# Kernel tuning notes

Measured on AMD Instinct MI355X. Metric: run time of the kernel, lower is better.

## Reference

```python
import jax, jax.numpy as jnp
import numpy as np

EPS = 1e-8
TAU = 1.0


def graph_conv(h_in, adj, W, b):
    # h: [N, D_out]
    h = h_in @ W
    nrm = jnp.linalg.norm(h, axis=1, keepdims=True)
    h_norm = h / jnp.maximum(nrm, EPS)  # F.normalize with eps clamp
    # cosine-sim logits + log-adjacency mask -> row softmax
    logits = (h_norm @ h_norm.T) / TAU + jnp.log(adj + EPS)  # [N, N]
    attn = jax.nn.softmax(logits, axis=1)
    return attn @ h + b


def setup_inputs() -> dict:
    key = jax.random.key(0)
    ks = jax.random.split(key, 20)
    N, F, H, C = 4096, 512, 128, 16

    def xavier(k, fan_in, fan_out):
        s = float(np.sqrt(6.0 / (fan_in + fan_out)))
        return jax.random.uniform(k, (fan_in, fan_out), minval=-s, maxval=s, dtype=jnp.float32)

    return {
        "x": jax.random.normal(ks[0], (N, F), dtype=jnp.float32),
        "adj_low": jax.random.uniform(ks[1], (N, N), dtype=jnp.float32),
        "adj_high": jax.random.uniform(ks[2], (N, N), dtype=jnp.float32),
        "adj_mid": jax.random.uniform(ks[3], (N, N), dtype=jnp.float32),
        "w_low0": xavier(ks[4], F, H), "b_low0": jnp.zeros((H,), jnp.float32),
        "w_high0": xavier(ks[5], F, H), "b_high0": jnp.zeros((H,), jnp.float32),
        "w_mid0": xavier(ks[6], F, H), "b_mid0": jnp.zeros((H,), jnp.float32),
        "w_low1": xavier(ks[7], H, C), "b_low1": jnp.zeros((C,), jnp.float32),
        "w_high1": xavier(ks[8], H, C), "b_high1": jnp.zeros((C,), jnp.float32),
        "w_mid1": xavier(ks[9], H, C), "b_mid1": jnp.zeros((C,), jnp.float32),
        "g0": jnp.ones((3,), jnp.float32),
        "g1": jnp.ones((3,), jnp.float32),
    }


def reference(x, adj_low, adj_high, adj_mid,
              w_low0, b_low0, w_high0, b_high0, w_mid0, b_mid0,
              w_low1, b_low1, w_high1, b_high1, w_mid1, b_mid1,
              g0, g1):
    # layer 0 (inner layer: ReLU; dropout p=0 in eval mode -> identity)
    hl = jax.nn.relu(graph_conv(x, adj_low, w_low0, b_low0))
    hh = jax.nn.relu(graph_conv(x, adj_high, w_high0, b_high0))
    hm = jax.nn.relu(graph_conv(x, adj_mid, w_mid0, b_mid0))
    w = jax.nn.softmax(g0)
    h = w[0] * hl + w[1] * hh + w[2] * hm

    # layer 1 (final layer: no activation)
    hl = graph_conv(h, adj_low, w_low1, b_low1)
    hh = graph_conv(h, adj_high, w_high1, b_high1)
    hm = graph_conv(h, adj_mid, w_mid1, b_mid1)
    w = jax.nn.softmax(g1)
    h = w[0] * hl + w[1] * hh + w[2] * hm

    return jax.nn.log_softmax(h, axis=-1)
```

## Files before the change

### kernel.cpp

```cpp
#include <hip/hip_runtime.h>

#define N_NODES 4096
#define F_IN 512
#define H_DIM 128
#define C_DIM 16
#define EPSF 1e-8f
#define LOG2E 1.4426950408889634f
#define SMAX 2.0f
#define NKS0 8
#define KLEN0 (N_NODES / NKS0)
#define NT0 (KLEN0 / 32)
#define NKS1 8

typedef __attribute__((ext_vector_type(8))) short bf16x8;
typedef __attribute__((ext_vector_type(4))) short bf16x4;
typedef __attribute__((ext_vector_type(4))) float f32x4;

__device__ __forceinline__ ushort f2bf(float f){
  union { float f; unsigned u; } v; v.f = f;
  unsigned u = v.u;
  return (ushort)((u + 0x7fffu + ((u >> 16) & 1u)) >> 16);
}
__device__ __forceinline__ float bf2f(ushort h){
  union { unsigned u; float f; } v; v.u = ((unsigned)h) << 16;
  return v.f;
}

__global__ __launch_bounds__(256) void proj0_kernel(
    const float* __restrict__ x,
    const float* __restrict__ Wl, const float* __restrict__ Wh,
    const float* __restrict__ Wm,
    ushort* __restrict__ hn, ushort* __restrict__ hvT)
{
  const int t = threadIdx.x;
  const int d = t & 127;
  const int half = t >> 7;
  const int r0 = blockIdx.x * 8;
  __shared__ float xs[8][F_IN];
  for (int i = t; i < 8 * F_IN; i += 256)
    xs[i >> 9][i & 511] = x[(size_t)(r0 + (i >> 9)) * F_IN + (i & 511)];
  __syncthreads();

  float acc0[8], acc1[8], acc2[8];
#pragma unroll
  for (int r = 0; r < 8; r++) { acc0[r] = 0.f; acc1[r] = 0.f; acc2[r] = 0.f; }

  const int k0 = half * (F_IN / 2);
  for (int k = k0; k < k0 + F_IN / 2; k++) {
    float wl = Wl[k * H_DIM + d];
    float wh = Wh[k * H_DIM + d];
    float wm = Wm[k * H_DIM + d];
#pragma unroll
    for (int r = 0; r < 8; r++) {
      float xv = xs[r][k];
      acc0[r] = fmaf(xv, wl, acc0[r]);
      acc1[r] = fmaf(xv, wh, acc1[r]);
      acc2[r] = fmaf(xv, wm, acc2[r]);
    }
  }

  __shared__ float part[3][8][128];
  if (half == 1) {
#pragma unroll
    for (int r = 0; r < 8; r++) {
      part[0][r][d] = acc0[r]; part[1][r][d] = acc1[r]; part[2][r][d] = acc2[r];
    }
  }
  __syncthreads();
  if (half == 0) {
#pragma unroll
    for (int r = 0; r < 8; r++) {
      acc0[r] += part[0][r][d]; acc1[r] += part[1][r][d]; acc2[r] += part[2][r][d];
    }
  }

  __shared__ float red[24][2];
  const int wv = t >> 6;
  const int lane = t & 63;

#define REDUCE_BRANCH(ACC, B)                                        \
  _Pragma("unroll")                                                  \
  for (int r = 0; r < 8; r++) {                                      \
    float v = ACC[r] * ACC[r];                                       \
    v += __shfl_down(v, 32); v += __shfl_down(v, 16);                \
    v += __shfl_down(v, 8);  v += __shfl_down(v, 4);                 \
    v += __shfl_down(v, 2);  v += __shfl_down(v, 1);                 \
    if (lane == 0) red[(B) * 8 + r][wv] = v;                         \
  }
  if (half == 0) {
    REDUCE_BRANCH(acc0, 0)
    REDUCE_BRANCH(acc1, 1)
    REDUCE_BRANCH(acc2, 2)
  }
  __syncthreads();

#define WRITE_BRANCH(ACC, B)                                                   \
  _Pragma("unroll")                                                            \
  for (int r = 0; r < 8; r++) {                                                \
    float nrm = sqrtf(red[(B) * 8 + r][0] + red[(B) * 8 + r][1]);              \
    float rn = 1.0f / fmaxf(nrm, EPSF);                                        \
    float h = ACC[r];                                                          \
    hn[((size_t)(B) * N_NODES + r0 + r) * H_DIM + d] = f2bf(h * rn);           \
    hvT[((size_t)(B) * H_DIM + d) * N_NODES + r0 + r] = f2bf(h);               \
  }
  if (half == 0) {
    WRITE_BRANCH(acc0, 0)
    WRITE_BRANCH(acc1, 1)
    WRITE_BRANCH(acc2, 2)
  }
#undef REDUCE_BRANCH
#undef WRITE_BRANCH
}

__global__ __launch_bounds__(512) void flash0_kernel(
    const ushort* __restrict__ hn, const ushort* __restrict__ hvT,
    const float* __restrict__ adj_l, const float* __restrict__ adj_h,
    const float* __restrict__ adj_m,
    float* __restrict__ pl0, ushort* __restrict__ pO)
{
  const int tid = threadIdx.x;
  const int w = tid >> 6;
  const int lane = tid & 63;
  const int lr = lane & 15;
  const int lg = lane >> 4;
  const int ks = blockIdx.y;
  const int b = blockIdx.z;
  const int q0 = blockIdx.x * 128 + w * 16;
  const float* adj = (b == 0) ? adj_l : (b == 1) ? adj_h : adj_m;
  const ushort* Qg = hn + (size_t)b * N_NODES * H_DIM;
  const ushort* VTg = hvT + (size_t)b * H_DIM * N_NODES;
  const int kbase = ks * KLEN0;

  __shared__ ushort sK[2][32 * 128];
  __shared__ ushort sV[2][128 * 32];
  __shared__ ushort pbuf[8][16][40];

  bf16x8 qf[4];
  {
    const ushort* qp = Qg + (size_t)(q0 + lr) * H_DIM + lg * 8;
#pragma unroll
    for (int u = 0; u < 4; u++) qf[u] = *(const bf16x8*)(qp + 32 * u);
  }

  f32x4 o[8];
#pragma unroll
  for (int dt = 0; dt < 8; dt++) o[dt] = (f32x4){0.f, 0.f, 0.f, 0.f};
  float lsum[4] = {0.f, 0.f, 0.f, 0.f};

  const int qrow_base = q0 + lg * 4;
  const float* ar[4];
#pragma unroll
  for (int r = 0; r < 4; r++)
    ar[r] = adj + (size_t)(qrow_base + r) * N_NODES + kbase;

  const int kk = tid >> 4, kc = tid & 15;
  const size_t kOff = (size_t)kk * H_DIM + ((size_t)(kc ^ (kk & 7)) << 3);
  const int dV = tid >> 2, vc = tid & 3;
  const size_t vOff = (size_t)dV * N_NODES + ((size_t)(vc ^ ((dV >> 1) & 3)) << 3);

#define STAGE(BUF, K0)                                                         \
  {                                                                            \
    const ushort* ksrc = Qg + (size_t)(K0) * H_DIM;                            \
    const ushort* vsrc = VTg + (K0);                                           \
    __builtin_amdgcn_global_load_lds(ksrc + kOff,                              \
        (char*)&sK[BUF][0] + w * 1024, 16, 0, 0);                              \
    __builtin_amdgcn_global_load_lds(vsrc + vOff,                              \
        (char*)&sV[BUF][0] + w * 1024, 16, 0, 0);                              \
  }

  STAGE(0, kbase)

  float a0c[4], a1c[4];
#pragma unroll
  for (int r = 0; r < 4; r++) { a0c[r] = ar[r][lr]; a1c[r] = ar[r][16 + lr]; }

  for (int t = 0; t < NT0; t++) {
    const int cur = t & 1;
    __syncthreads();
    if (t + 1 < NT0) STAGE(cur ^ 1, kbase + (t + 1) * 32)

    float a0n[4], a1n[4];
    if (t + 1 < NT0) {
#pragma unroll
      for (int r = 0; r < 4; r++) {
        a0n[r] = ar[r][(t + 1) * 32 + lr];
        a1n[r] = ar[r][(t + 1) * 32 + 16 + lr];
      }
    }

    f32x4 s0 = (f32x4){0.f, 0.f, 0.f, 0.f};
    f32x4 s1 = (f32x4){0.f, 0.f, 0.f, 0.f};
    const char* sKc = (const char*)&sK[cur][0];
#pragma unroll
    for (int u = 0; u < 4; u++) {
      const int c0 = lg + 4 * u;
      bf16x8 kf0 = *(const bf16x8*)(sKc + lr * 256 + ((c0 ^ (lr & 7)) << 4));
      bf16x8 kf1 = *(const bf16x8*)(sKc + (lr + 16) * 256 + ((c0 ^ (lr & 7)) << 4));
      s0 = __builtin_amdgcn_mfma_f32_16x16x32_bf16(qf[u], kf0, s0, 0, 0, 0);
      s1 = __builtin_amdgcn_mfma_f32_16x16x32_bf16(qf[u], kf1, s1, 0, 0, 0);
    }
    float p0[4], p1[4];
#pragma unroll
    for (int r = 0; r < 4; r++) {
      float e0 = exp2f(fmaf(s0[r], LOG2E, -SMAX));
      float e1 = exp2f(fmaf(s1[r], LOG2E, -SMAX));
      p0[r] = e0 * (a0c[r] + EPSF);
      p1[r] = e1 * (a1c[r] + EPSF);
      lsum[r] += p0[r] + p1[r];
    }
#pragma unroll
    for (int r = 0; r < 4; r++) {
      pbuf[w][lg * 4 + r][lr]      = f2bf(p0[r]);
      pbuf[w][lg * 4 + r][16 + lr] = f2bf(p1[r]);
    }
    bf16x8 pf = *(const bf16x8*)&pbuf[w][lr][lg * 8];
    const char* sVc = (const char*)&sV[cur][0];
#pragma unroll
    for (int dt = 0; dt < 8; dt++) {
      const int dd = dt * 16 + lr;
      bf16x8 vf = *(const bf16x8*)(sVc + dd * 64 + ((lg ^ ((dd >> 1) & 3)) << 4));
      o[dt] = __builtin_amdgcn_mfma_f32_16x16x32_bf16(pf, vf, o[dt], 0, 0, 0);
    }
#pragma unroll
    for (int r = 0; r < 4; r++) { a0c[r] = a0n[r]; a1c[r] = a1n[r]; }
  }
#undef STAGE

  const int ps = b * NKS0 + ks;
#pragma unroll
  for (int r = 0; r < 4; r++) {
    const size_t row = (size_t)ps * N_NODES + qrow_base + r;
    float psum = lsum[r];
#pragma unroll
    for (int dd = 1; dd < 16; dd <<= 1) psum += __shfl_xor(psum, dd);
    if (lr == 0) pl0[row] = psum;
#pragma unroll
    for (int dt = 0; dt < 8; dt++)
      pO[row * H_DIM + dt * 16 + lr] = f2bf(o[dt][r]);
  }
}

__global__ __launch_bounds__(128) void mix1_kernel(
    const float* __restrict__ pl0, const ushort* __restrict__ pO,
    const float* __restrict__ bl0, const float* __restrict__ bh0,
    const float* __restrict__ bm0,
    const float* __restrict__ Wl1, const float* __restrict__ Wh1,
    const float* __restrict__ Wm1,
    const float* __restrict__ g0,
    ushort* __restrict__ hn1b, ushort* __restrict__ hbT)
{
  const int q = blockIdx.x;
  const int t = threadIdx.x;
  float ga = g0[0], gb = g0[1], gc = g0[2];
  float gm = fmaxf(ga, fmaxf(gb, gc));
  float e0 = expf(ga - gm), e1 = expf(gb - gm), e2 = expf(gc - gm);
  float ei = 1.0f / (e0 + e1 + e2);

  __shared__ float Ls[3];
  if (t < 3) {
    float L = 0.f;
#pragma unroll
    for (int ks = 0; ks < NKS0; ks++) L += pl0[(size_t)(t * NKS0 + ks) * N_NODES + q];
    Ls[t] = L;
  }
  float O0 = 0.f, O1 = 0.f, O2 = 0.f;
#pragma unroll
  for (int ks = 0; ks < NKS0; ks++) {
    O0 += bf2f(pO[((size_t)(0 * NKS0 + ks) * N_NODES + q) * H_DIM + t]);
    O1 += bf2f(pO[((size_t)(1 * NKS0 + ks) * N_NODES + q) * H_DIM + t]);
    O2 += bf2f(pO[((size_t)(2 * NKS0 + ks) * N_NODES + q) * H_DIM + t]);
  }
  __syncthreads();

  __shared__ float hc[H_DIM];
  hc[t] = e0 * ei * fmaxf(O0 / Ls[0] + bl0[t], 0.f)
        + e1 * ei * fmaxf(O1 / Ls[1] + bh0[t], 0.f)
        + e2 * ei * fmaxf(O2 / Ls[2] + bm0[t], 0.f);
  __syncthreads();

  __shared__ float shb[48];
  if (t < 48) {
    const int b = t >> 4, j = t & 15;
    const float* W = (b == 0) ? Wl1 : (b == 1) ? Wh1 : Wm1;
    float s = 0.f;
    for (int k = 0; k < H_DIM; k++) s = fmaf(hc[k], W[k * C_DIM + j], s);
    shb[t] = s;
  }
  __syncthreads();
  __shared__ float rns[3];
  if (t < 3) {
    float s = 0.f;
#pragma unroll
    for (int j = 0; j < C_DIM; j++) { float u = shb[t * C_DIM + j]; s = fmaf(u, u, s); }
    rns[t] = 1.0f / fmaxf(sqrtf(s), EPSF);
  }
  __syncthreads();
  if (t < 48) {
    const int b = t >> 4, j = t & 15;
    hbT[((size_t)b * C_DIM + j) * N_NODES + q] = f2bf(shb[t]);
    hn1b[((size_t)b * N_NODES + q) * C_DIM + j] = f2bf(shb[t] * rns[b]);
  }
}

__global__ __launch_bounds__(256) void flash1_kernel(
    const ushort* __restrict__ hn1b, const ushort* __restrict__ hbT,
    const float* __restrict__ adj_l, const float* __restrict__ adj_h,
    const float* __restrict__ adj_m,
    float* __restrict__ pl, float* __restrict__ pacc)
{
  const int tid = threadIdx.x;
  const int wid = tid >> 6;
  const int lane = tid & 63;
  const int lr = lane & 15;
  const int lg = lane >> 4;
  const int qblk = blockIdx.x * 64;
  const int q0 = qblk + wid * 16;
  const int ks = blockIdx.y;
  const int b = blockIdx.z;
  const float* adj = (b == 0) ? adj_l : (b == 1) ? adj_h : adj_m;
  const ushort* Qn = hn1b + (size_t)b * N_NODES * C_DIM;
  const ushort* VT = hbT + (size_t)b * C_DIM * N_NODES;
  const int kbase = ks * (N_NODES / NKS1);
  const int nt = (N_NODES / NKS1) / 32;

  __shared__ float sAdj[2][64 * 32];

  const bf16x4 qf = *(const bf16x4*)(Qn + (size_t)(q0 + lr) * C_DIM + lg * 4);
  const f32x4 zero = (f32x4){0.f, 0.f, 0.f, 0.f};
  f32x4 o = zero;
  float lsum = 0.f;
  const ushort* vrow = VT + (size_t)lr * N_NODES;

  const int rowA = tid >> 3, cA = tid & 7;
  const int rowB = rowA + 32;
  const size_t aOffA = (size_t)rowA * N_NODES + ((size_t)(cA ^ (rowA & 7)) << 2);
  const size_t aOffB = (size_t)rowB * N_NODES + ((size_t)(cA ^ (rowB & 7)) << 2);
  const float* adjq = adj + (size_t)qblk * N_NODES;

#define STAGE1(BUF, K0)                                                        \
  {                                                                            \
    const float* asrc = adjq + (K0);                                           \
    __builtin_amdgcn_global_load_lds(asrc + aOffA,                             \
        (char*)&sAdj[BUF][0] + wid * 1024, 16, 0, 0);                          \
    __builtin_amdgcn_global_load_lds(asrc + aOffB,                             \
        (char*)&sAdj[BUF][0] + 4096 + wid * 1024, 16, 0, 0);                   \
  }

  STAGE1(0, kbase)

  const int rowL = wid * 16 + lr;
  const int adr0 = rowL * 32 + ((lg ^ (rowL & 7)) << 2);
  const int adr1 = rowL * 32 + (((4 + lg) ^ (rowL & 7)) << 2);

  for (int t = 0; t < nt; t++) {
    const int cur = t & 1;
    __syncthreads();
    if (t + 1 < nt) STAGE1(cur ^ 1, kbase + (t + 1) * 32)

    const int k0 = kbase + t * 32;
    bf16x4 kf0 = *(const bf16x4*)(Qn + (size_t)(k0 + lr) * C_DIM + lg * 4);
    bf16x4 kf1 = *(const bf16x4*)(Qn + (size_t)(k0 + 16 + lr) * C_DIM + lg * 4);
    f32x4 s0 = __builtin_amdgcn_mfma_f32_16x16x16bf16_1k(kf0, qf, zero, 0, 0, 0);
    f32x4 s1 = __builtin_amdgcn_mfma_f32_16x16x16bf16_1k(kf1, qf, zero, 0, 0, 0);
    f32x4 a0 = *(const f32x4*)&sAdj[cur][adr0];
    f32x4 a1 = *(const f32x4*)&sAdj[cur][adr1];
    bf16x4 pf0, pf1;
#pragma unroll
    for (int r = 0; r < 4; r++) {
      float e0 = exp2f(fmaf(s0[r], LOG2E, -SMAX));
      float e1 = exp2f(fmaf(s1[r], LOG2E, -SMAX));
      float p0 = e0 * (a0[r] + EPSF);
      float p1 = e1 * (a1[r] + EPSF);
      lsum += p0 + p1;
      pf0[r] = (short)f2bf(p0);
      pf1[r] = (short)f2bf(p1);
    }
    bf16x4 vf0 = *(const bf16x4*)(vrow + k0 + lg * 4);
    bf16x4 vf1 = *(const bf16x4*)(vrow + k0 + 16 + lg * 4);
    o = __builtin_amdgcn_mfma_f32_16x16x16bf16_1k(pf0, vf0, o, 0, 0, 0);
    o = __builtin_amdgcn_mfma_f32_16x16x16bf16_1k(pf1, vf1, o, 0, 0, 0);
  }
#undef STAGE1

  const int ps = b * NKS1 + ks;
  float psum = lsum;
  psum += __shfl_xor(psum, 16);
  psum += __shfl_xor(psum, 32);
  if (lg == 0) pl[(size_t)ps * N_NODES + q0 + lr] = psum;
#pragma unroll
  for (int r = 0; r < 4; r++)
    pacc[((size_t)ps * N_NODES + q0 + lg * 4 + r) * C_DIM + lr] = o[r];
}

__global__ __launch_bounds__(256) void combine1_kernel(
    const float* __restrict__ pl, const float* __restrict__ pacc,
    float* __restrict__ o1)
{
  const int q = blockIdx.x * 256 + threadIdx.x;
  const int b = blockIdx.y;
  float L = 0.f;
  f32x4 out0 = (f32x4){0,0,0,0}, out1 = (f32x4){0,0,0,0},
        out2 = (f32x4){0,0,0,0}, out3 = (f32x4){0,0,0,0};
#pragma unroll
  for (int ks = 0; ks < NKS1; ks++) {
    const size_t pidx = (size_t)(b * NKS1 + ks) * N_NODES + q;
    L += pl[pidx];
    const f32x4* pa = (const f32x4*)(pacc + pidx * C_DIM);
    out0 += pa[0]; out1 += pa[1]; out2 += pa[2]; out3 += pa[3];
  }
  float invL = 1.0f / L;
  f32x4* dst = (f32x4*)(o1 + ((size_t)b * N_NODES + q) * C_DIM);
  dst[0] = out0 * invL; dst[1] = out1 * invL; dst[2] = out2 * invL; dst[3] = out3 * invL;
}

__global__ __launch_bounds__(256) void final_kernel(
    const float* __restrict__ o1,
    const float* __restrict__ bl1, const float* __restrict__ bh1,
    const float* __restrict__ bm1,
    const float* __restrict__ g1, float* __restrict__ out)
{
  const int q = blockIdx.x * 256 + threadIdx.x;
  float ga = g1[0], gb = g1[1], gc = g1[2];
  float gm = fmaxf(ga, fmaxf(gb, gc));
  float e0 = expf(ga - gm), e1 = expf(gb - gm), e2 = expf(gc - gm);
  float ei = 1.0f / (e0 + e1 + e2);
  float w0 = e0 * ei, w1 = e1 * ei, w2 = e2 * ei;
  const size_t NC = (size_t)N_NODES * C_DIM;

  float v[16];
#pragma unroll
  for (int i = 0; i < 4; i++) {
    f32x4 a = ((const f32x4*)(o1 + (size_t)q * C_DIM))[i];
    f32x4 bA = ((const f32x4*)(o1 + NC + (size_t)q * C_DIM))[i];
    f32x4 c = ((const f32x4*)(o1 + 2 * NC + (size_t)q * C_DIM))[i];
    f32x4 xl = ((const f32x4*)bl1)[i];
    f32x4 xh = ((const f32x4*)bh1)[i];
    f32x4 xm = ((const f32x4*)bm1)[i];
#pragma unroll
    for (int j = 0; j < 4; j++)
      v[i * 4 + j] = w0 * (a[j] + xl[j]) + w1 * (bA[j] + xh[j]) + w2 * (c[j] + xm[j]);
  }
  float mx = -1e30f;
#pragma unroll
  for (int j = 0; j < 16; j++) mx = fmaxf(mx, v[j]);
  float se = 0.f;
#pragma unroll
  for (int j = 0; j < 16; j++) se += expf(v[j] - mx);
  float lse = mx + logf(se);
  f32x4* dst = (f32x4*)(out + (size_t)q * C_DIM);
#pragma unroll
  for (int i = 0; i < 4; i++) {
    f32x4 r;
#pragma unroll
    for (int j = 0; j < 4; j++) r[j] = v[i * 4 + j] - lse;
    dst[i] = r;
  }
}

extern "C" void kernel_launch(void* const* d_in, const int* in_sizes, int n_in,
                              void* d_out, int out_size, void* d_ws, size_t ws_size,
                              hipStream_t stream) {
  (void)in_sizes; (void)n_in; (void)out_size; (void)ws_size;
  const float* x     = (const float*)d_in[0];
  const float* adj_l = (const float*)d_in[1];
  const float* adj_h = (const float*)d_in[2];
  const float* adj_m = (const float*)d_in[3];
  const float* w_l0  = (const float*)d_in[4];
  const float* b_l0  = (const float*)d_in[5];
  const float* w_h0  = (const float*)d_in[6];
  const float* b_h0  = (const float*)d_in[7];
  const float* w_m0  = (const float*)d_in[8];
  const float* b_m0  = (const float*)d_in[9];
  const float* w_l1  = (const float*)d_in[10];
  const float* b_l1  = (const float*)d_in[11];
  const float* w_h1  = (const float*)d_in[12];
  const float* b_h1  = (const float*)d_in[13];
  const float* w_m1  = (const float*)d_in[14];
  const float* b_m1  = (const float*)d_in[15];
  const float* g0    = (const float*)d_in[16];
  const float* g1    = (const float*)d_in[17];
  float* out = (float*)d_out;

  char* ws = (char*)d_ws;
  ushort* hn  = (ushort*)(ws);
  ushort* hvT = (ushort*)(ws + (3u << 20));
  ushort* hn1b= (ushort*)(ws + (6u << 20));
  ushort* hbT = (ushort*)(ws + (6u << 20) + (384u << 10));
  float*  pl0 = (float*)(ws + (12u << 20));
  ushort* pO  = (ushort*)(ws + (12u << 20) + (512u << 10));
  float*  pl  = (float*)(ws + (12u << 20));
  float*  pacc= (float*)(ws + (13u << 20));
  float*  o1  = (float*)(ws + (20u << 20));

  proj0_kernel<<<dim3(512), dim3(256), 0, stream>>>(x, w_l0, w_h0, w_m0, hn, hvT);
  flash0_kernel<<<dim3(32, NKS0, 3), dim3(512), 0, stream>>>(hn, hvT, adj_l, adj_h, adj_m,
                                                             pl0, pO);
  mix1_kernel<<<dim3(4096), dim3(128), 0, stream>>>(pl0, pO, b_l0, b_h0, b_m0,
                                                    w_l1, w_h1, w_m1, g0, hn1b, hbT);
  flash1_kernel<<<dim3(64, NKS1, 3), dim3(256), 0, stream>>>(hn1b, hbT, adj_l, adj_h, adj_m,
                                                             pl, pacc);
  combine1_kernel<<<dim3(16, 3), dim3(256), 0, stream>>>(pl, pacc, o1);
  final_kernel<<<dim3(16), dim3(256), 0, stream>>>(o1, b_l1, b_h1, b_m1, g1, out);
}
```

Baseline: 160.5 us.

## Process two 16-row query tiles per wave in flash0 with 256-thread blocks

Halves the flash0 block to 4 waves, with each wave now handling 32 query rows as two 16-row MFMA tiles. Each K/V fragment read from LDS therefore feeds twice as many MFMAs, which cuts LDS read traffic per FLOP. Each thread now issues two global_load_lds per buffer to cover the same staging. The software prefetch of adjacency values one iteration ahead was removed in favour of loading them in the same iteration, and register pressure roughly doubles for accumulators, so occupancy and latency hiding may drop.

After: 170.7 us. +6.4%, slower.

```diff
diff --git a/kernel.cpp b/kernel.cpp
--- a/kernel.cpp
+++ b/kernel.cpp
@@ -112,7 +112,7 @@
 #undef WRITE_BRANCH
 }
 
-__global__ __launch_bounds__(512) void flash0_kernel(
+__global__ __launch_bounds__(256) void flash0_kernel(
     const ushort* __restrict__ hn, const ushort* __restrict__ hvT,
     const float* __restrict__ adj_l, const float* __restrict__ adj_h,
     const float* __restrict__ adj_m,
@@ -125,7 +125,7 @@
   const int lg = lane >> 4;
   const int ks = blockIdx.y;
   const int b = blockIdx.z;
-  const int q0 = blockIdx.x * 128 + w * 16;
+  const int q0 = blockIdx.x * 128 + w * 32;
   const float* adj = (b == 0) ? adj_l : (b == 1) ? adj_h : adj_m;
   const ushort* Qg = hn + (size_t)b * N_NODES * H_DIM;
   const ushort* VTg = hvT + (size_t)b * H_DIM * N_NODES;
@@ -133,110 +133,141 @@
 
   __shared__ ushort sK[2][32 * 128];
   __shared__ ushort sV[2][128 * 32];
-  __shared__ ushort pbuf[8][16][40];
-
-  bf16x8 qf[4];
+  __shared__ ushort pbuf[4][2][16][40];
+
+  bf16x8 qfA[4], qfB[4];
   {
-    const ushort* qp = Qg + (size_t)(q0 + lr) * H_DIM + lg * 8;
-#pragma unroll
-    for (int u = 0; u < 4; u++) qf[u] = *(const bf16x8*)(qp + 32 * u);
-  }
-
-  f32x4 o[8];
-#pragma unroll
-  for (int dt = 0; dt < 8; dt++) o[dt] = (f32x4){0.f, 0.f, 0.f, 0.f};
-  float lsum[4] = {0.f, 0.f, 0.f, 0.f};
-
-  const int qrow_base = q0 + lg * 4;
-  const float* ar[4];
-#pragma unroll
-  for (int r = 0; r < 4; r++)
-    ar[r] = adj + (size_t)(qrow_base + r) * N_NODES + kbase;
-
-  const int kk = tid >> 4, kc = tid & 15;
-  const size_t kOff = (size_t)kk * H_DIM + ((size_t)(kc ^ (kk & 7)) << 3);
-  const int dV = tid >> 2, vc = tid & 3;
-  const size_t vOff = (size_t)dV * N_NODES + ((size_t)(vc ^ ((dV >> 1) & 3)) << 3);
+    const ushort* qpA = Qg + (size_t)(q0 + lr) * H_DIM + lg * 8;
+    const ushort* qpB = qpA + 16 * H_DIM;
+#pragma unroll
+    for (int u = 0; u < 4; u++) {
+      qfA[u] = *(const bf16x8*)(qpA + 32 * u);
+      qfB[u] = *(const bf16x8*)(qpB + 32 * u);
+    }
+  }
+
+  f32x4 oA[8], oB[8];
+#pragma unroll
+  for (int dt = 0; dt < 8; dt++) {
+    oA[dt] = (f32x4){0.f, 0.f, 0.f, 0.f};
+    oB[dt] = (f32x4){0.f, 0.f, 0.f, 0.f};
+  }
+  float lsA[4] = {0.f, 0.f, 0.f, 0.f};
+  float lsB[4] = {0.f, 0.f, 0.f, 0.f};
+
+  const int qrA = q0 + lg * 4;
+  const int qrB = q0 + 16 + lg * 4;
+  const float* arA[4];
+  const float* arB[4];
+#pragma unroll
+  for (int r = 0; r < 4; r++) {
+    arA[r] = adj + (size_t)(qrA + r) * N_NODES + kbase;
+    arB[r] = adj + (size_t)(qrB + r) * N_NODES + kbase;
+  }
+
+  const int sA = w * 128 + lane;
+  const int sB = sA + 64;
+  const int kkA = sA >> 4, kcA = sA & 15;
+  const int kkB = sB >> 4, kcB = sB & 15;
+  const size_t kOffA = (size_t)kkA * H_DIM + ((size_t)(kcA ^ (kkA & 7)) << 3);
+  const size_t kOffB = (size_t)kkB * H_DIM + ((size_t)(kcB ^ (kkB & 7)) << 3);
+  const int dA = sA >> 2, vcA = sA & 3;
+  const int dB = sB >> 2, vcB = sB & 3;
+  const size_t vOffA = (size_t)dA * N_NODES + ((size_t)(vcA ^ ((dA >> 1) & 3)) << 3);
+  const size_t vOffB = (size_t)dB * N_NODES + ((size_t)(vcB ^ ((dB >> 1) & 3)) << 3);
 
 #define STAGE(BUF, K0)                                                         \
   {                                                                            \
     const ushort* ksrc = Qg + (size_t)(K0) * H_DIM;                            \
     const ushort* vsrc = VTg + (K0);                                           \
-    __builtin_amdgcn_global_load_lds(ksrc + kOff,                              \
-        (char*)&sK[BUF][0] + w * 1024, 16, 0, 0);                              \
-    __builtin_amdgcn_global_load_lds(vsrc + vOff,                              \
-        (char*)&sV[BUF][0] + w * 1024, 16, 0, 0);                              \
+    __builtin_amdgcn_global_load_lds(ksrc + kOffA,                             \
+        (char*)&sK[BUF][0] + w * 2048, 16, 0, 0);                              \
+    __builtin_amdgcn_global_load_lds(ksrc + kOffB,                             \
+        (char*)&sK[BUF][0] + w * 2048 + 1024, 16, 0, 0);                       \
+    __builtin_amdgcn_global_load_lds(vsrc + vOffA,                             \
+        (char*)&sV[BUF][0] + w * 2048, 16, 0, 0);                              \
+    __builtin_amdgcn_global_load_lds(vsrc + vOffB,                             \
+        (char*)&sV[BUF][0] + w * 2048 + 1024, 16, 0, 0);                       \
   }
 
   STAGE(0, kbase)
-
-  float a0c[4], a1c[4];
-#pragma unroll
-  for (int r = 0; r < 4; r++) { a0c[r] = ar[r][lr]; a1c[r] = ar[r][16 + lr]; }
 
   for (int t = 0; t < NT0; t++) {
     const int cur = t & 1;
     __syncthreads();
     if (t + 1 < NT0) STAGE(cur ^ 1, kbase + (t + 1) * 32)
 
-    float a0n[4], a1n[4];
-    if (t + 1 < NT0) {
-#pragma unroll
-      for (int r = 0; r < 4; r++) {
-        a0n[r] = ar[r][(t + 1) * 32 + lr];
-        a1n[r] = ar[r][(t + 1) * 32 + 16 + lr];
-      }
-    }
-
-    f32x4 s0 = (f32x4){0.f, 0.f, 0.f, 0.f};
-    f32x4 s1 = (f32x4){0.f, 0.f, 0.f, 0.f};
+    float aA0[4], aA1[4], aB0[4], aB1[4];
+#pragma unroll
+    for (int r = 0; r < 4; r++) {
+      aA0[r] = arA[r][t * 32 + lr];
+      aA1[r] = arA[r][t * 32 + 16 + lr];
+      aB0[r] = arB[r][t * 32 + lr];
+      aB1[r] = arB[r][t * 32 + 16 + lr];
+    }
+
+    f32x4 sA0 = (f32x4){0.f, 0.f, 0.f, 0.f};
+    f32x4 sA1 = (f32x4){0.f, 0.f, 0.f, 0.f};
+    f32x4 sB0 = (f32x4){0.f, 0.f, 0.f, 0.f};
+    f32x4 sB1 = (f32x4){0.f, 0.f, 0.f, 0.f};
     const char* sKc = (const char*)&sK[cur][0];
 #pragma unroll
     for (int u = 0; u < 4; u++) {
       const int c0 = lg + 4 * u;
       bf16x8 kf0 = *(const bf16x8*)(sKc + lr * 256 + ((c0 ^ (lr & 7)) << 4));
       bf16x8 kf1 = *(const bf16x8*)(sKc + (lr + 16) * 256 + ((c0 ^ (lr & 7)) << 4));
-      s0 = __builtin_amdgcn_mfma_f32_16x16x32_bf16(qf[u], kf0, s0, 0, 0, 0);
-      s1 = __builtin_amdgcn_mfma_f32_16x16x32_bf16(qf[u], kf1, s1, 0, 0, 0);
-    }
-    float p0[4], p1[4];
+      sA0 = __builtin_amdgcn_mfma_f32_16x16x32_bf16(qfA[u], kf0, sA0, 0, 0, 0);
+      sA1 = __builtin_amdgcn_mfma_f32_16x16x32_bf16(qfA[u], kf1, sA1, 0, 0, 0);
+      sB0 = __builtin_amdgcn_mfma_f32_16x16x32_bf16(qfB[u], kf0, sB0, 0, 0, 0);
+      sB1 = __builtin_amdgcn_mfma_f32_16x16x32_bf16(qfB[u], kf1, sB1, 0, 0, 0);
+    }
+    float pA0[4], pA1[4], pB0[4], pB1[4];
 #pragma unroll
     for (int r = 0; r < 4; r++) {
-      float e0 = exp2f(fmaf(s0[r], LOG2E, -SMAX));
-      float e1 = exp2f(fmaf(s1[r], LOG2E, -SMAX));
-      p0[r] = e0 * (a0c[r] + EPSF);
-      p1[r] = e1 * (a1c[r] + EPSF);
-      lsum[r] += p0[r] + p1[r];
+      pA0[r] = exp2f(fmaf(sA0[r], LOG2E, -SMAX)) * (aA0[r] + EPSF);
+      pA1[r] = exp2f(fmaf(sA1[r], LOG2E, -SMAX)) * (aA1[r] + EPSF);
+      pB0[r] = exp2f(fmaf(sB0[r], LOG2E, -SMAX)) * (aB0[r] + EPSF);
+      pB1[r] = exp2f(fmaf(sB1[r], LOG2E, -SMAX)) * (aB1[r] + EPSF);
+      lsA[r] += pA0[r] + pA1[r];
+      lsB[r] += pB0[r] + pB1[r];
     }
 #pragma unroll
     for (int r = 0; r < 4; r++) {
-      pbuf[w][lg * 4 + r][lr]      = f2bf(p0[r]);
-      pbuf[w][lg * 4 + r][16 + lr] = f2bf(p1[r]);
-    }
-    bf16x8 pf = *(const bf16x8*)&pbuf[w][lr][lg * 8];
+      pbuf[w][0][lg * 4 + r][lr]      = f2bf(pA0[r]);
+      pbuf[w][0][lg * 4 + r][16 + lr] = f2bf(pA1[r]);
+      pbuf[w][1][lg * 4 + r][lr]      = f2bf(pB0[r]);
+      pbuf[w][1][lg * 4 + r][16 + lr] = f2bf(pB1[r]);
+    }
+    bf16x8 pfA = *(const bf16x8*)&pbuf[w][0][lr][lg * 8];
+    bf16x8 pfB = *(const bf16x8*)&pbuf[w][1][lr][lg * 8];
     const char* sVc = (const char*)&sV[cur][0];
 #pragma unroll
     for (int dt = 0; dt < 8; dt++) {
       const int dd = dt * 16 + lr;
       bf16x8 vf = *(const bf16x8*)(sVc + dd * 64 + ((lg ^ ((dd >> 1) & 3)) << 4));
-      o[dt] = __builtin_amdgcn_mfma_f32_16x16x32_bf16(pf, vf, o[dt], 0, 0, 0);
-    }
-#pragma unroll
-    for (int r = 0; r < 4; r++) { a0c[r] = a0n[r]; a1c[r] = a1n[r]; }
+      oA[dt] = __builtin_amdgcn_mfma_f32_16x16x32_bf16(pfA, vf, oA[dt], 0, 0, 0);
+      oB[dt] = __builtin_amdgcn_mfma_f32_16x16x32_bf16(pfB, vf, oB[dt], 0, 0, 0);
+    }
   }
 #undef STAGE
 
   const int ps = b * NKS0 + ks;
 #pragma unroll
   for (int r = 0; r < 4; r++) {
-    const size_t row = (size_t)ps * N_NODES + qrow_base + r;
-    float psum = lsum[r];
-#pragma unroll
-    for (int dd = 1; dd < 16; dd <<= 1) psum += __shfl_xor(psum, dd);
-    if (lr == 0) pl0[row] = psum;
-#pragma unroll
-    for (int dt = 0; dt < 8; dt++)
-      pO[row * H_DIM + dt * 16 + lr] = f2bf(o[dt][r]);
+    const size_t rowA = (size_t)ps * N_NODES + qrA + r;
+    const size_t rowB = (size_t)ps * N_NODES + qrB + r;
+    float psA = lsA[r], psB = lsB[r];
+#pragma unroll
+    for (int dd = 1; dd < 16; dd <<= 1) {
+      psA += __shfl_xor(psA, dd);
+      psB += __shfl_xor(psB, dd);
+    }
+    if (lr == 0) { pl0[rowA] = psA; pl0[rowB] = psB; }
+#pragma unroll
+    for (int dt = 0; dt < 8; dt++) {
+      pO[rowA * H_DIM + dt * 16 + lr] = f2bf(oA[dt][r]);
+      pO[rowB * H_DIM + dt * 16 + lr] = f2bf(oB[dt][r]);
+    }
   }
 }
 
@@ -493,7 +524,7 @@
   float*  o1  = (float*)(ws + (20u << 20));
 
   proj0_kernel<<<dim3(512), dim3(256), 0, stream>>>(x, w_l0, w_h0, w_m0, hn, hvT);
-  flash0_kernel<<<dim3(32, NKS0, 3), dim3(512), 0, stream>>>(hn, hvT, adj_l, adj_h, adj_m,
+  flash0_kernel<<<dim3(32, NKS0, 3), dim3(256), 0, stream>>>(hn, hvT, adj_l, adj_h, adj_m,
                                                              pl0, pO);
   mix1_kernel<<<dim3(4096), dim3(128), 0, stream>>>(pl0, pO, b_l0, b_h0, b_m0,
                                                     w_l1, w_h1, w_m1, g0, hn1b, hbT);
```

## Compute transposed scores in flash0 to keep P in registers, drop LDS round-trip

Applied to the files above, without the earlier changes.

Swaps the MFMA operand order so each lane holds score columns for a single query row, which lets the probabilities feed the PV MFMA directly as bf16x4 fragments using 16x16x16 instructions. This removes the per-wave pbuf LDS staging and the scalar adjacency loads, replacing them with vectorized f32x4 loads of the adjacency row. The block also shrinks from 512 to 256 threads (64 query rows) with each thread issuing two async K/V loads per stage, doubling grid size. The trade-off is twice as many PV MFMA instructions at half K depth, and adjacency loads are no longer prefetched one tile ahead.

Result: slower. 168.3 us (+4.9%).

```diff
diff --git a/kernel.cpp b/kernel.cpp
--- a/kernel.cpp
+++ b/kernel.cpp
@@ -112,7 +112,7 @@
 #undef WRITE_BRANCH
 }
 
-__global__ __launch_bounds__(512) void flash0_kernel(
+__global__ __launch_bounds__(256) void flash0_kernel(
     const ushort* __restrict__ hn, const ushort* __restrict__ hvT,
     const float* __restrict__ adj_l, const float* __restrict__ adj_h,
     const float* __restrict__ adj_m,
@@ -125,7 +125,7 @@
   const int lg = lane >> 4;
   const int ks = blockIdx.y;
   const int b = blockIdx.z;
-  const int q0 = blockIdx.x * 128 + w * 16;
+  const int q0 = blockIdx.x * 64 + w * 16;
   const float* adj = (b == 0) ? adj_l : (b == 1) ? adj_h : adj_m;
   const ushort* Qg = hn + (size_t)b * N_NODES * H_DIM;
   const ushort* VTg = hvT + (size_t)b * H_DIM * N_NODES;
@@ -133,7 +133,6 @@
 
   __shared__ ushort sK[2][32 * 128];
   __shared__ ushort sV[2][128 * 32];
-  __shared__ ushort pbuf[8][16][40];
 
   bf16x8 qf[4];
   {
@@ -145,48 +144,44 @@
   f32x4 o[8];
 #pragma unroll
   for (int dt = 0; dt < 8; dt++) o[dt] = (f32x4){0.f, 0.f, 0.f, 0.f};
-  float lsum[4] = {0.f, 0.f, 0.f, 0.f};
-
-  const int qrow_base = q0 + lg * 4;
-  const float* ar[4];
-#pragma unroll
-  for (int r = 0; r < 4; r++)
-    ar[r] = adj + (size_t)(qrow_base + r) * N_NODES + kbase;
-
-  const int kk = tid >> 4, kc = tid & 15;
-  const size_t kOff = (size_t)kk * H_DIM + ((size_t)(kc ^ (kk & 7)) << 3);
-  const int dV = tid >> 2, vc = tid & 3;
-  const size_t vOff = (size_t)dV * N_NODES + ((size_t)(vc ^ ((dV >> 1) & 3)) << 3);
+  float lsum = 0.f;
+
+  const float* arow = adj + (size_t)(q0 + lr) * N_NODES + kbase;
+
+  const int sA = w * 128 + lane;
+  const int sB = sA + 64;
+  const int kkA = sA >> 4, kcA = sA & 15;
+  const int kkB = sB >> 4, kcB = sB & 15;
+  const size_t kOffA = (size_t)kkA * H_DIM + ((size_t)(kcA ^ (kkA & 7)) << 3);
+  const size_t kOffB = (size_t)kkB * H_DIM + ((size_t)(kcB ^ (kkB & 7)) << 3);
+  const int dA = sA >> 2, vcA = sA & 3;
+  const int dB = sB >> 2, vcB = sB & 3;
+  const size_t vOffA = (size_t)dA * N_NODES + ((size_t)(vcA ^ ((dA >> 1) & 3)) << 3);
+  const size_t vOffB = (size_t)dB * N_NODES + ((size_t)(vcB ^ ((dB >> 1) & 3)) << 3);
 
 #define STAGE(BUF, K0)                                                         \
   {                                                                            \
     const ushort* ksrc = Qg + (size_t)(K0) * H_DIM;                            \
     const ushort* vsrc = VTg + (K0);                                           \
-    __builtin_amdgcn_global_load_lds(ksrc + kOff,                              \
-        (char*)&sK[BUF][0] + w * 1024, 16, 0, 0);                              \
-    __builtin_amdgcn_global_load_lds(vsrc + vOff,                              \
-        (char*)&sV[BUF][0] + w * 1024, 16, 0, 0);                              \
+    __builtin_amdgcn_global_load_lds(ksrc + kOffA,                             \
+        (char*)&sK[BUF][0] + w * 2048, 16, 0, 0);                              \
+    __builtin_amdgcn_global_load_lds(ksrc + kOffB,                             \
+        (char*)&sK[BUF][0] + w * 2048 + 1024, 16, 0, 0);                       \
+    __builtin_amdgcn_global_load_lds(vsrc + vOffA,                             \
+        (char*)&sV[BUF][0] + w * 2048, 16, 0, 0);                              \
+    __builtin_amdgcn_global_load_lds(vsrc + vOffB,                             \
+        (char*)&sV[BUF][0] + w * 2048 + 1024, 16, 0, 0);                       \
   }
 
   STAGE(0, kbase)
-
-  float a0c[4], a1c[4];
-#pragma unroll
-  for (int r = 0; r < 4; r++) { a0c[r] = ar[r][lr]; a1c[r] = ar[r][16 + lr]; }
 
   for (int t = 0; t < NT0; t++) {
     const int cur = t & 1;
     __syncthreads();
     if (t + 1 < NT0) STAGE(cur ^ 1, kbase + (t + 1) * 32)
 
-    float a0n[4], a1n[4];
-    if (t + 1 < NT0) {
-#pragma unroll
-      for (int r = 0; r < 4; r++) {
-        a0n[r] = ar[r][(t + 1) * 32 + lr];
-        a1n[r] = ar[r][(t + 1) * 32 + 16 + lr];
-      }
-    }
+    f32x4 a0 = *(const f32x4*)(arow + t * 32 + lg * 4);
+    f32x4 a1 = *(const f32x4*)(arow + t * 32 + 16 + lg * 4);
 
     f32x4 s0 = (f32x4){0.f, 0.f, 0.f, 0.f};
     f32x4 s1 = (f32x4){0.f, 0.f, 0.f, 0.f};
@@ -196,47 +191,45 @@
       const int c0 = lg + 4 * u;
       bf16x8 kf0 = *(const bf16x8*)(sKc + lr * 256 + ((c0 ^ (lr & 7)) << 4));
       bf16x8 kf1 = *(const bf16x8*)(sKc + (lr + 16) * 256 + ((c0 ^ (lr & 7)) << 4));
-      s0 = __builtin_amdgcn_mfma_f32_16x16x32_bf16(qf[u], kf0, s0, 0, 0, 0);
-      s1 = __builtin_amdgcn_mfma_f32_16x16x32_bf16(qf[u], kf1, s1, 0, 0, 0);
-    }
-    float p0[4], p1[4];
+      s0 = __builtin_amdgcn_mfma_f32_16x16x32_bf16(kf0, qf[u], s0, 0, 0, 0);
+      s1 = __builtin_amdgcn_mfma_f32_16x16x32_bf16(kf1, qf[u], s1, 0, 0, 0);
+    }
+    bf16x4 pf0, pf1;
 #pragma unroll
     for (int r = 0; r < 4; r++) {
-      float e0 = exp2f(fmaf(s0[r], LOG2E, -SMAX));
-      float e1 = exp2f(fmaf(s1[r], LOG2E, -SMAX));
-      p0[r] = e0 * (a0c[r] + EPSF);
-      p1[r] = e1 * (a1c[r] + EPSF);
-      lsum[r] += p0[r] + p1[r];
-    }
-#pragma unroll
-    for (int r = 0; r < 4; r++) {
-      pbuf[w][lg * 4 + r][lr]      = f2bf(p0[r]);
-      pbuf[w][lg * 4 + r][16 + lr] = f2bf(p1[r]);
-    }
-    bf16x8 pf = *(const bf16x8*)&pbuf[w][lr][lg * 8];
+      float p0 = exp2f(fmaf(s0[r], LOG2E, -SMAX)) * (a0[r] + EPSF);
+      float p1 = exp2f(fmaf(s1[r], LOG2E, -SMAX)) * (a1[r] + EPSF);
+      lsum += p0 + p1;
+      pf0[r] = (short)f2bf(p0);
+      pf1[r] = (short)f2bf(p1);
+    }
     const char* sVc = (const char*)&sV[cur][0];
 #pragma unroll
     for (int dt = 0; dt < 8; dt++) {
       const int dd = dt * 16 + lr;
-      bf16x8 vf = *(const bf16x8*)(sVc + dd * 64 + ((lg ^ ((dd >> 1) & 3)) << 4));
-      o[dt] = __builtin_amdgcn_mfma_f32_16x16x32_bf16(pf, vf, o[dt], 0, 0, 0);
-    }
-#pragma unroll
-    for (int r = 0; r < 4; r++) { a0c[r] = a0n[r]; a1c[r] = a1n[r]; }
+      const int sw = (dd >> 1) & 3;
+      bf16x4 vf0 = *(const bf16x4*)(sVc + dd * 64 +
+                     ((((lg >> 1) + 0) ^ sw) << 4) + (lg & 1) * 8);
+      bf16x4 vf1 = *(const bf16x4*)(sVc + dd * 64 +
+                     ((((lg >> 1) + 2) ^ sw) << 4) + (lg & 1) * 8);
+      o[dt] = __builtin_amdgcn_mfma_f32_16x16x16bf16_1k(pf0, vf0, o[dt], 0, 0, 0);
+      o[dt] = __builtin_amdgcn_mfma_f32_16x16x16bf16_1k(pf1, vf1, o[dt], 0, 0, 0);
+    }
   }
 #undef STAGE
 
   const int ps = b * NKS0 + ks;
-#pragma unroll
-  for (int r = 0; r < 4; r++) {
-    const size_t row = (size_t)ps * N_NODES + qrow_base + r;
-    float psum = lsum[r];
-#pragma unroll
-    for (int dd = 1; dd < 16; dd <<= 1) psum += __shfl_xor(psum, dd);
-    if (lr == 0) pl0[row] = psum;
-#pragma unroll
-    for (int dt = 0; dt < 8; dt++)
-      pO[row * H_DIM + dt * 16 + lr] = f2bf(o[dt][r]);
+  float psum = lsum;
+  psum += __shfl_xor(psum, 16);
+  psum += __shfl_xor(psum, 32);
+  if (lg == 0) pl0[(size_t)ps * N_NODES + q0 + lr] = psum;
+#pragma unroll
+  for (int dt = 0; dt < 8; dt++) {
+#pragma unroll
+    for (int r = 0; r < 4; r++) {
+      pO[((size_t)ps * N_NODES + q0 + lg * 4 + r) * H_DIM + dt * 16 + lr] =
+          f2bf(o[dt][r]);
+    }
   }
 }
 
@@ -493,7 +486,7 @@
   float*  o1  = (float*)(ws + (20u << 20));
 
   proj0_kernel<<<dim3(512), dim3(256), 0, stream>>>(x, w_l0, w_h0, w_m0, hn, hvT);
-  flash0_kernel<<<dim3(32, NKS0, 3), dim3(512), 0, stream>>>(hn, hvT, adj_l, adj_h, adj_m,
+  flash0_kernel<<<dim3(64, NKS0, 3), dim3(256), 0, stream>>>(hn, hvT, adj_l, adj_h, adj_m,
                                                              pl0, pO);
   mix1_kernel<<<dim3(4096), dim3(128), 0, stream>>>(pl0, pO, b_l0, b_h0, b_m0,
                                                     w_l1, w_h1, w_m1, g0, hn1b, hbT);
```
